# Kernel optimization log

Measured on AMD Instinct MI355X. Metric: run time of the kernel, lower is better.

Reference implementation:

```python
import jax, jax.numpy as jnp
import numpy as np

N = 50000      # nodes
E = 800000     # edges
D_IN = 128     # raw feature dim
H = 96         # hidden_channels
K = 8          # experts
L = 4          # num_layers
C = 40         # classes


def setup_inputs() -> dict:
    key = jax.random.key(0)
    ks = jax.random.split(key, 10)
    stdv = 1.0 / np.sqrt(H)
    inp = {
        'x': jax.random.normal(ks[0], (N, D_IN), dtype=jnp.float32),
        'edge_index': jax.random.randint(ks[1], (2, E), 0, N, dtype=jnp.int64),
        # fcs[0]: Linear(d, hidden); fcs[1]: Linear(hidden, c)
        'fc0_w': jax.random.normal(ks[2], (D_IN, H), dtype=jnp.float32) * 0.05,
        'fc0_b': jnp.zeros((H,), dtype=jnp.float32),
        'fc1_w': jax.random.normal(ks[3], (H, C), dtype=jnp.float32) * 0.05,
        'fc1_b': jnp.zeros((C,), dtype=jnp.float32),
        # context_enc (method='node'): per-layer Linear(hidden, K)
        'ctx_w': jax.random.normal(ks[4], (L, H, K), dtype=jnp.float32) * 0.05,
        'ctx_b': jnp.zeros((L, K), dtype=jnp.float32),
        # GraphMultiConvolution weights: [L, K, hidden, hidden], uniform(-stdv, stdv)
        'conv_w': jax.random.uniform(ks[5], (L, K, H, H), dtype=jnp.float32,
                                     minval=-stdv, maxval=stdv),
    }
    return inp


def reference(x, edge_index, fc0_w, fc0_b, fc1_w, fc1_b, ctx_w, ctx_b, conv_w):
    # eval-mode forward (training=False): no dropout, softmax routing
    row = edge_index[0]
    col = edge_index[1]
    h = jax.nn.relu(x @ fc0_w + fc0_b)                     # [N, H]
    for i in range(L):
        # routing logits and soft expert weights z: [N, K]
        z = jax.nn.softmax(h @ ctx_w[i] + ctx_b[i], axis=-1)
        # spmm aggregation: hi[r] = sum over edges (r, c) of h[c]
        hi = jax.ops.segment_sum(h[col], row, num_segments=N)  # [N, H]
        # K-expert batched matmul: [N, K, H]
        outs = jnp.einsum('nd,kdo->nko', hi, conv_w[i])
        # gumbel/softmax-weighted combine + residual
        out = jnp.einsum('nk,nko->no', z, outs) + h
        h = jax.nn.relu(out)
    return h @ fc1_w + fc1_b                               # [N, C]
```

## Files before the change

kernel.cpp:

```cpp
#include <hip/hip_runtime.h>

#define N_NODES 50000
#define N_EDGES 800000
#define DIN     128
#define H       96
#define K_EXP   8
#define L_LAYERS 4
#define C_OUT   40

typedef _Float16 f16;
typedef f16 f16x2 __attribute__((ext_vector_type(2)));
typedef f16 f16x4 __attribute__((ext_vector_type(4)));
typedef f16 f16x8 __attribute__((ext_vector_type(8)));
typedef float f32x4 __attribute__((ext_vector_type(4)));


#define CONV_TOT (L_LAYERS * K_EXP * H * H)
#define FC0_TOT  (DIN * H)
#define FC1_TOT  (48 * H)
#define CNT_BLOCKS ((N_EDGES + 255) / 256)
#define CVT_BLOCKS ((CONV_TOT + FC0_TOT + FC1_TOT + 255) / 256)

__global__ __launch_bounds__(256) void count_convert(const int* __restrict__ row,
                                                     int* __restrict__ deg,
                                                     int* __restrict__ p,
                                                     const float* __restrict__ conv_w,
                                                     const float* __restrict__ fc0_w,
                                                     const float* __restrict__ fc1_w,
                                                     f16* __restrict__ wfrag,
                                                     f16* __restrict__ fc0t,
                                                     f16* __restrict__ fc1t) {
    int tid = threadIdx.x;
    if ((int)blockIdx.x < CNT_BLOCKS) {
        int i = blockIdx.x * 256 + tid;
        if (i < N_EDGES) p[i] = atomicAdd(&deg[row[i]], 1);
    } else {
        int i = ((int)blockIdx.x - CNT_BLOCKS) * 256 + tid;
        if (i < CONV_TOT) {
            int o = i % H;
            int t = i / H;
            int d = t % H;
            int lk = t / H;
            int ct = o >> 4, lc = o & 15;
            int ks = d >> 5, quad = (d >> 3) & 3, j = d & 7;
            wfrag[(size_t)lk * 9216 + ct * 1536 + ks * 512 + (quad * 16 + lc) * 8 + j] =
                (f16)conv_w[i];
        } else if (i < CONV_TOT + FC0_TOT) {
            int j = i - CONV_TOT;
            int o = j % H, d = j / H;
            fc0t[o * DIN + d] = (f16)fc0_w[j];
        } else if (i < CONV_TOT + FC0_TOT + FC1_TOT) {
            int j = i - CONV_TOT - FC0_TOT;
            int o = j / H, d = j % H;
            fc1t[j] = (o < C_OUT) ? (f16)fc1_w[d * C_OUT + o] : (f16)0.f;
        }
    }
}

__global__ __launch_bounds__(1024) void scanA(const int* __restrict__ deg,
                                              int* __restrict__ rowptr,
                                              int* __restrict__ partial, int n) {
    __shared__ int wsum[16];
    int tid  = threadIdx.x;
    int lane = tid & 63, wid = tid >> 6;
    int idx = blockIdx.x * 1024 + tid;
    int v = (idx < n) ? deg[idx] : 0;
    int s = v;
    #pragma unroll
    for (int off = 1; off < 64; off <<= 1) {
        int t = __shfl_up(s, off, 64);
        if (lane >= off) s += t;
    }
    if (lane == 63) wsum[wid] = s;
    __syncthreads();
    if (wid == 0 && lane < 16) {
        int w = wsum[lane];
        #pragma unroll
        for (int off = 1; off < 16; off <<= 1) {
            int t = __shfl_up(w, off, 16);
            if (lane >= off) w += t;
        }
        wsum[lane] = w;
    }
    __syncthreads();
    int waveoff = (wid == 0) ? 0 : wsum[wid - 1];
    if (idx < n) rowptr[idx + 1] = waveoff + s;
    if (tid == 1023) partial[blockIdx.x] = waveoff + s;
}

__global__ __launch_bounds__(1024) void scanC(int* __restrict__ rowptr,
                                              const int* __restrict__ partial,
                                              int nb, int n) {
    __shared__ int boff_s;
    int tid = threadIdx.x;
    if (tid < 64) {
        int v = 0;
        for (int j = tid; j < (int)blockIdx.x; j += 64) v += partial[j];
        #pragma unroll
        for (int off = 32; off >= 1; off >>= 1) v += __shfl_xor(v, off, 64);
        if (tid == 0) boff_s = v;
    }
    __syncthreads();
    int boff = boff_s;
    int idx = blockIdx.x * 1024 + tid;
    if (idx == 0) rowptr[0] = 0;
    if (idx < n) rowptr[idx + 1] += boff;
}


#define SCT_BLOCKS 1024
#define FPAD 136

__global__ __launch_bounds__(256) void scatter_fc0(const int* __restrict__ row,
                                                   const int* __restrict__ col,
                                                   const int* __restrict__ p,
                                                   const int* __restrict__ rowptr,
                                                   int* __restrict__ csr,
                                                   const float* __restrict__ x,
                                                   const f16* __restrict__ fc0t,
                                                   const float* __restrict__ b,
                                                   f16* __restrict__ h16, int n) {
    __shared__ f16 As[64 * FPAD];
    __shared__ f16 Ws[96 * FPAD];
    int tid = threadIdx.x;
    if ((int)blockIdx.x < SCT_BLOCKS) {
        int stride = SCT_BLOCKS * 256;
        for (int i = blockIdx.x * 256 + tid; i < N_EDGES; i += stride)
            csr[rowptr[row[i]] + p[i]] = col[i];
        return;
    }
    int l = tid & 63, w = tid >> 6;
    int quad = l >> 4, lc = l & 15;
    int row0 = ((int)blockIdx.x - SCT_BLOCKS) * 64;

    for (int t = tid; t < 2048; t += 256) {
        int m = t >> 5, c4 = (t & 31) * 4;
        int gr = row0 + m;
        float4 v = {0.f, 0.f, 0.f, 0.f};
        if (gr < n) v = *(const float4*)(x + (size_t)gr * DIN + c4);
        f16x4 h4 = {(f16)v.x, (f16)v.y, (f16)v.z, (f16)v.w};
        *(f16x4*)&As[m * FPAD + c4] = h4;
    }
    for (int t = tid; t < 1536; t += 256) {
        int o = t >> 4, c8 = (t & 15) * 8;
        *(f16x8*)&Ws[o * FPAD + c8] = *(const f16x8*)(fc0t + o * DIN + c8);
    }
    __syncthreads();

    f16x8 afr[4];
    #pragma unroll
    for (int ks = 0; ks < 4; ks++)
        afr[ks] = *(const f16x8*)&As[(16 * w + lc) * FPAD + ks * 32 + quad * 8];

    f32x4 acc[6] = {};
    #pragma unroll
    for (int ct = 0; ct < 6; ct++) {
        #pragma unroll
        for (int ks = 0; ks < 4; ks++) {
            f16x8 bfr = *(const f16x8*)&Ws[(ct * 16 + lc) * FPAD + ks * 32 + quad * 8];
            acc[ct] = __builtin_amdgcn_mfma_f32_16x16x32_f16(afr[ks], bfr, acc[ct], 0, 0, 0);
        }
    }

    int m0 = 16 * w + quad * 4;
    #pragma unroll
    for (int r = 0; r < 4; r++) {
        int gr = row0 + m0 + r;
        if (gr < n) {
            #pragma unroll
            for (int ct = 0; ct < 6; ct++) {
                int o = ct * 16 + lc;
                h16[(size_t)gr * H + o] = (f16)fmaxf(acc[ct][r] + b[o], 0.f);
            }
        }
    }
}


#define LF_ROWS   64
#define LF_BLOCKS ((N_NODES + LF_ROWS - 1) / LF_ROWS)
#define HPAD      104

#define ACC8(v) { _Pragma("unroll") for (int q = 0; q < 8; q++) acc[q] += (float)(v)[q]; }

__global__ __launch_bounds__(256, 4) void layer_fused(const f16* __restrict__ h16,
                                                      const int* __restrict__ rowptr,
                                                      const int* __restrict__ csr,
                                                      const float* __restrict__ cw,
                                                      const float* __restrict__ cb,
                                                      const f16* __restrict__ wfrag,
                                                      f16* __restrict__ hout16, int n) {
    __shared__ f16 hi_lds[LF_ROWS * HPAD];
    __shared__ f16 Wl[9216];
    __shared__ float ws[H * K_EXP];
    __shared__ f16 z_lds[LF_ROWS * K_EXP];
    __shared__ float bs[K_EXP];

    int tid = threadIdx.x;
    int brow = blockIdx.x * LF_ROWS;

    for (int t = tid; t < H * K_EXP; t += 256) ws[t] = cw[t];
    if (tid < K_EXP) bs[tid] = cb[tid];

    {
        int g = tid >> 4, li = tid & 15;
        bool act = li < 12;
        const f16* hb = h16 + li * 8;
        for (int sub = 0; sub < 4; sub++) {
            int r = brow + g * 4 + sub;
            if (r >= n) break;
            int j = rowptr[r], e = rowptr[r + 1];
            float acc[8] = {};
            int4 qa = *(const int4*)(csr + j);
            int4 qb = *(const int4*)(csr + j + 4);
            while (j + 8 <= e) {
                int4 na = *(const int4*)(csr + j + 8);
                int4 nb = *(const int4*)(csr + j + 12);
                f16x8 v0 = {}, v1 = {}, v2 = {}, v3 = {}, v4 = {}, v5 = {}, v6 = {}, v7 = {};
                if (act) {
                    v0 = *(const f16x8*)(hb + (size_t)qa.x * H);
                    v1 = *(const f16x8*)(hb + (size_t)qa.y * H);
                    v2 = *(const f16x8*)(hb + (size_t)qa.z * H);
                    v3 = *(const f16x8*)(hb + (size_t)qa.w * H);
                    v4 = *(const f16x8*)(hb + (size_t)qb.x * H);
                    v5 = *(const f16x8*)(hb + (size_t)qb.y * H);
                    v6 = *(const f16x8*)(hb + (size_t)qb.z * H);
                    v7 = *(const f16x8*)(hb + (size_t)qb.w * H);
                }
                ACC8(v0) ACC8(v1) ACC8(v2) ACC8(v3)
                ACC8(v4) ACC8(v5) ACC8(v6) ACC8(v7)
                j += 8; qa = na; qb = nb;
            }
            if (j + 4 <= e) {
                f16x8 v0 = {}, v1 = {}, v2 = {}, v3 = {};
                if (act) {
                    v0 = *(const f16x8*)(hb + (size_t)qa.x * H);
                    v1 = *(const f16x8*)(hb + (size_t)qa.y * H);
                    v2 = *(const f16x8*)(hb + (size_t)qa.z * H);
                    v3 = *(const f16x8*)(hb + (size_t)qa.w * H);
                }
                ACC8(v0) ACC8(v1) ACC8(v2) ACC8(v3)
                j += 4; qa = qb;
            }
            int rem = e - j;
            if (rem > 0) {
                f16x8 v0 = {}, v1 = {}, v2 = {};
                if (act) {
                    v0 = *(const f16x8*)(hb + (size_t)qa.x * H);
                    if (rem > 1) v1 = *(const f16x8*)(hb + (size_t)qa.y * H);
                    if (rem > 2) v2 = *(const f16x8*)(hb + (size_t)qa.z * H);
                }
                ACC8(v0)
                if (rem > 1) ACC8(v1)
                if (rem > 2) ACC8(v2)
            }
            if (act) {
                f16x8 o;
                #pragma unroll
                for (int q = 0; q < 8; q++) o[q] = (f16)acc[q];
                *(f16x8*)&hi_lds[(g * 4 + sub) * HPAD + li * 8] = o;
            }
        }
    }

    __syncthreads();
    if (tid < LF_ROWS) {
        int node = brow + tid;
        if (node < n) {
            float acc[K_EXP];
            #pragma unroll
            for (int k = 0; k < K_EXP; k++) acc[k] = bs[k];
            const f16* hr = h16 + (size_t)node * H;
            #pragma unroll 3
            for (int c8 = 0; c8 < 12; c8++) {
                f16x8 v = *(const f16x8*)(hr + c8 * 8);
                #pragma unroll
                for (int j = 0; j < 8; j++) {
                    float hv = (float)v[j];
                    int d = c8 * 8 + j;
                    #pragma unroll
                    for (int k = 0; k < K_EXP; k++) acc[k] += hv * ws[d * K_EXP + k];
                }
            }
            float mx = acc[0];
            #pragma unroll
            for (int k = 1; k < K_EXP; k++) mx = fmaxf(mx, acc[k]);
            float s = 0.f;
            #pragma unroll
            for (int k = 0; k < K_EXP; k++) { acc[k] = __expf(acc[k] - mx); s += acc[k]; }
            float inv = 1.f / s;
            f16x8 zo;
            #pragma unroll
            for (int k = 0; k < K_EXP; k++) zo[k] = (f16)(acc[k] * inv);
            *(f16x8*)&z_lds[tid * K_EXP] = zo;
        }
    }
    __syncthreads();

    int l = tid & 63, w = tid >> 6;
    int quad = l >> 4, lc = l & 15;

    f16x8 afr[3];
    #pragma unroll
    for (int ks = 0; ks < 3; ks++)
        afr[ks] = *(const f16x8*)&hi_lds[(w * 16 + lc) * HPAD + ks * 32 + quad * 8];
    f16x8 zh = *(const f16x8*)&z_lds[(w * 16 + lc) * K_EXP];

    f32x4 acc[6] = {};
    for (int k = 0; k < K_EXP; k++) {
        if (k) __syncthreads();
        const f16* src = wfrag + (size_t)k * 9216;
        for (int t = tid; t < 1152; t += 256)
            *(f16x8*)&Wl[t * 8] = *(const f16x8*)(src + t * 8);
        __syncthreads();

        f16 s = zh[k];
        f16x8 as0 = afr[0] * s, as1 = afr[1] * s, as2 = afr[2] * s;
        #pragma unroll
        for (int ct = 0; ct < 6; ct++) {
            f16x8 b0 = *(const f16x8*)&Wl[ct * 1536 + 0 * 512 + l * 8];
            f16x8 b1 = *(const f16x8*)&Wl[ct * 1536 + 1 * 512 + l * 8];
            f16x8 b2 = *(const f16x8*)&Wl[ct * 1536 + 2 * 512 + l * 8];
            acc[ct] = __builtin_amdgcn_mfma_f32_16x16x32_f16(as0, b0, acc[ct], 0, 0, 0);
            acc[ct] = __builtin_amdgcn_mfma_f32_16x16x32_f16(as1, b1, acc[ct], 0, 0, 0);
            acc[ct] = __builtin_amdgcn_mfma_f32_16x16x32_f16(as2, b2, acc[ct], 0, 0, 0);
        }
    }

    #pragma unroll
    for (int r = 0; r < 4; r++) {
        int gr = brow + w * 16 + quad * 4 + r;
        if (gr < n) {
            #pragma unroll
            for (int ct = 0; ct < 6; ct++) {
                int o = ct * 16 + lc;
                float v = fmaxf(acc[ct][r] + (float)h16[(size_t)gr * H + o], 0.f);
                hout16[(size_t)gr * H + o] = (f16)v;
            }
        }
    }
}


#define APAD 104

__global__ __launch_bounds__(256) void fc1_kernel(const f16* __restrict__ h16,
                                                  const f16* __restrict__ fc1t,
                                                  const float* __restrict__ b,
                                                  float* __restrict__ out, int n) {
    __shared__ f16 As[64 * APAD];
    __shared__ f16 Ws[48 * APAD];
    int tid = threadIdx.x;
    int l = tid & 63, w = tid >> 6;
    int quad = l >> 4, lc = l & 15;
    int row0 = blockIdx.x * 64;

    for (int t = tid; t < 768; t += 256) {
        int m = t / 12, c8 = (t % 12) * 8;
        int gr = row0 + m;
        f16x8 v = {};
        if (gr < n) v = *(const f16x8*)(h16 + (size_t)gr * H + c8);
        *(f16x8*)&As[m * APAD + c8] = v;
    }
    for (int t = tid; t < 576; t += 256) {
        int o = t / 12, c8 = (t % 12) * 8;
        *(f16x8*)&Ws[o * APAD + c8] = *(const f16x8*)(fc1t + o * H + c8);
    }
    __syncthreads();

    f16x8 afr[3];
    #pragma unroll
    for (int ks = 0; ks < 3; ks++)
        afr[ks] = *(const f16x8*)&As[(16 * w + lc) * APAD + ks * 32 + quad * 8];

    f32x4 acc[3] = {};
    #pragma unroll
    for (int ct = 0; ct < 3; ct++) {
        #pragma unroll
        for (int ks = 0; ks < 3; ks++) {
            f16x8 bfr = *(const f16x8*)&Ws[(ct * 16 + lc) * APAD + ks * 32 + quad * 8];
            acc[ct] = __builtin_amdgcn_mfma_f32_16x16x32_f16(afr[ks], bfr, acc[ct], 0, 0, 0);
        }
    }

    int m0 = 16 * w + quad * 4;
    #pragma unroll
    for (int r = 0; r < 4; r++) {
        int gr = row0 + m0 + r;
        if (gr < n) {
            #pragma unroll
            for (int ct = 0; ct < 3; ct++) {
                int o = ct * 16 + lc;
                if (o < C_OUT)
                    out[(size_t)gr * C_OUT + o] = acc[ct][r] + b[o];
            }
        }
    }
}


extern "C" void kernel_launch(void* const* d_in, const int* in_sizes, int n_in,
                              void* d_out, int out_size, void* d_ws, size_t ws_size,
                              hipStream_t stream) {
    const float* x      = (const float*)d_in[0];
    const int*   ei     = (const int*)d_in[1];
    const float* fc0_w  = (const float*)d_in[2];
    const float* fc0_b  = (const float*)d_in[3];
    const float* fc1_w  = (const float*)d_in[4];
    const float* fc1_b  = (const float*)d_in[5];
    const float* ctx_w  = (const float*)d_in[6];
    const float* ctx_b  = (const float*)d_in[7];
    const float* conv_w = (const float*)d_in[8];
    float* out = (float*)d_out;

    const size_t NH = (size_t)N_NODES * H;

    f16*   h16a = (f16*)d_ws;
    f16*   h16b = h16a + NH;
    f16*   wfrag= h16b + NH;
    f16*   fc0t = wfrag + CONV_TOT;
    f16*   fc1t = fc0t + FC0_TOT;
    int* rowptr = (int*)(fc1t + FC1_TOT);
    int* deg    = rowptr + (N_NODES + 1);
    int* csr    = deg + N_NODES;
    int* prank  = csr + N_EDGES;
    int* partial  = prank + N_EDGES;

    const int* row = ei;
    const int* col = ei + N_EDGES;

    hipMemsetAsync(deg, 0, sizeof(int) * N_NODES, stream);

    count_convert<<<CNT_BLOCKS + CVT_BLOCKS, 256, 0, stream>>>(
        row, deg, prank, conv_w, fc0_w, fc1_w, wfrag, fc0t, fc1t);
    int nsb = (N_NODES + 1023) / 1024;
    scanA<<<nsb, 1024, 0, stream>>>(deg, rowptr, partial, N_NODES);
    scanC<<<nsb, 1024, 0, stream>>>(rowptr, partial, nsb, N_NODES);

    int gemm_grid = (N_NODES + 63) / 64;
    scatter_fc0<<<SCT_BLOCKS + gemm_grid, 256, 0, stream>>>(
        row, col, prank, rowptr, csr, x, fc0t, fc0_b, h16a, N_NODES);

    f16* hcur = h16a;
    f16* hnext = h16b;
    for (int i = 0; i < L_LAYERS; i++) {
        layer_fused<<<LF_BLOCKS, 256, 0, stream>>>(
            hcur, rowptr, csr,
            ctx_w + (size_t)i * H * K_EXP, ctx_b + (size_t)i * K_EXP,
            wfrag + (size_t)i * K_EXP * H * H, hnext, N_NODES);
        f16* t = hcur; hcur = hnext; hnext = t;
    }
    fc1_kernel<<<gemm_grid, 256, 0, stream>>>(hcur, fc1t, fc1_b, out, N_NODES);
}
```

Before: 336.8 us.

## Make layer_fused wave-independent: per-wave gather, shuffle softmax, direct global weight loads

Restructures the fused layer kernel so each wavefront handles its own 16 rows end to end. The sparse gather rows are remapped per wave, and the routing softmax is computed by all 64 lanes with cross-quad shuffles instead of a single 64-thread group writing to LDS. Expert weight fragments are read straight from global/L2 instead of being staged through a 9216-element LDS buffer with block-wide barriers per expert. The smaller LDS footprint lets the occupancy hint rise from 4 to 6 blocks, at the cost of repeated global weight traffic per wave and more register pressure from the fully unrolled expert loop.

```diff
diff --git a/kernel.cpp b/kernel.cpp
--- a/kernel.cpp
+++ b/kernel.cpp
@@ -183,7 +183,7 @@
 
 #define ACC8(v) { _Pragma("unroll") for (int q = 0; q < 8; q++) acc[q] += (float)(v)[q]; }
 
-__global__ __launch_bounds__(256, 4) void layer_fused(const f16* __restrict__ h16,
+__global__ __launch_bounds__(256, 6) void layer_fused(const f16* __restrict__ h16,
                                                       const int* __restrict__ rowptr,
                                                       const int* __restrict__ csr,
                                                       const float* __restrict__ cw,
@@ -191,9 +191,7 @@
                                                       const f16* __restrict__ wfrag,
                                                       f16* __restrict__ hout16, int n) {
     __shared__ f16 hi_lds[LF_ROWS * HPAD];
-    __shared__ f16 Wl[9216];
     __shared__ float ws[H * K_EXP];
-    __shared__ f16 z_lds[LF_ROWS * K_EXP];
     __shared__ float bs[K_EXP];
 
     int tid = threadIdx.x;
@@ -201,140 +199,142 @@
 
     for (int t = tid; t < H * K_EXP; t += 256) ws[t] = cw[t];
     if (tid < K_EXP) bs[tid] = cb[tid];
+    __syncthreads();
+
+    int l = tid & 63, w = tid >> 6;
+    int quad = l >> 4, li = l & 15;
+    int wrow = brow + w * 16;
+    if (wrow >= n) return;
 
     {
-        int g = tid >> 4, li = tid & 15;
         bool act = li < 12;
         const f16* hb = h16 + li * 8;
         for (int sub = 0; sub < 4; sub++) {
-            int r = brow + g * 4 + sub;
-            if (r >= n) break;
-            int j = rowptr[r], e = rowptr[r + 1];
+            int r = wrow + quad * 4 + sub;
             float acc[8] = {};
-            int4 qa = *(const int4*)(csr + j);
-            int4 qb = *(const int4*)(csr + j + 4);
-            while (j + 8 <= e) {
-                int4 na = *(const int4*)(csr + j + 8);
-                int4 nb = *(const int4*)(csr + j + 12);
-                f16x8 v0 = {}, v1 = {}, v2 = {}, v3 = {}, v4 = {}, v5 = {}, v6 = {}, v7 = {};
-                if (act) {
-                    v0 = *(const f16x8*)(hb + (size_t)qa.x * H);
-                    v1 = *(const f16x8*)(hb + (size_t)qa.y * H);
-                    v2 = *(const f16x8*)(hb + (size_t)qa.z * H);
-                    v3 = *(const f16x8*)(hb + (size_t)qa.w * H);
-                    v4 = *(const f16x8*)(hb + (size_t)qb.x * H);
-                    v5 = *(const f16x8*)(hb + (size_t)qb.y * H);
-                    v6 = *(const f16x8*)(hb + (size_t)qb.z * H);
-                    v7 = *(const f16x8*)(hb + (size_t)qb.w * H);
+            if (r < n) {
+                int j = rowptr[r], e = rowptr[r + 1];
+                int4 qa = *(const int4*)(csr + j);
+                int4 qb = *(const int4*)(csr + j + 4);
+                while (j + 8 <= e) {
+                    int4 na = *(const int4*)(csr + j + 8);
+                    int4 nb = *(const int4*)(csr + j + 12);
+                    f16x8 v0 = {}, v1 = {}, v2 = {}, v3 = {}, v4 = {}, v5 = {}, v6 = {}, v7 = {};
+                    if (act) {
+                        v0 = *(const f16x8*)(hb + (size_t)qa.x * H);
+                        v1 = *(const f16x8*)(hb + (size_t)qa.y * H);
+                        v2 = *(const f16x8*)(hb + (size_t)qa.z * H);
+                        v3 = *(const f16x8*)(hb + (size_t)qa.w * H);
+                        v4 = *(const f16x8*)(hb + (size_t)qb.x * H);
+                        v5 = *(const f16x8*)(hb + (size_t)qb.y * H);
+                        v6 = *(const f16x8*)(hb + (size_t)qb.z * H);
+                        v7 = *(const f16x8*)(hb + (size_t)qb.w * H);
+                    }
+                    ACC8(v0) ACC8(v1) ACC8(v2) ACC8(v3)
+                    ACC8(v4) ACC8(v5) ACC8(v6) ACC8(v7)
+                    j += 8; qa = na; qb = nb;
                 }
-                ACC8(v0) ACC8(v1) ACC8(v2) ACC8(v3)
-                ACC8(v4) ACC8(v5) ACC8(v6) ACC8(v7)
-                j += 8; qa = na; qb = nb;
-            }
-            if (j + 4 <= e) {
-                f16x8 v0 = {}, v1 = {}, v2 = {}, v3 = {};
-                if (act) {
-                    v0 = *(const f16x8*)(hb + (size_t)qa.x * H);
-                    v1 = *(const f16x8*)(hb + (size_t)qa.y * H);
-                    v2 = *(const f16x8*)(hb + (size_t)qa.z * H);
-                    v3 = *(const f16x8*)(hb + (size_t)qa.w * H);
+                if (j + 4 <= e) {
+                    f16x8 v0 = {}, v1 = {}, v2 = {}, v3 = {};
+                    if (act) {
+                        v0 = *(const f16x8*)(hb + (size_t)qa.x * H);
+                        v1 = *(const f16x8*)(hb + (size_t)qa.y * H);
+                        v2 = *(const f16x8*)(hb + (size_t)qa.z * H);
+                        v3 = *(const f16x8*)(hb + (size_t)qa.w * H);
+                    }
+                    ACC8(v0) ACC8(v1) ACC8(v2) ACC8(v3)
+                    j += 4; qa = qb;
                 }
-                ACC8(v0) ACC8(v1) ACC8(v2) ACC8(v3)
-                j += 4; qa = qb;
-            }
-            int rem = e - j;
-            if (rem > 0) {
-                f16x8 v0 = {}, v1 = {}, v2 = {};
-                if (act) {
-                    v0 = *(const f16x8*)(hb + (size_t)qa.x * H);
-                    if (rem > 1) v1 = *(const f16x8*)(hb + (size_t)qa.y * H);
-                    if (rem > 2) v2 = *(const f16x8*)(hb + (size_t)qa.z * H);
+                int rem = e - j;
+                if (rem > 0) {
+                    f16x8 v0 = {}, v1 = {}, v2 = {};
+                    if (act) {
+                        v0 = *(const f16x8*)(hb + (size_t)qa.x * H);
+                        if (rem > 1) v1 = *(const f16x8*)(hb + (size_t)qa.y * H);
+                        if (rem > 2) v2 = *(const f16x8*)(hb + (size_t)qa.z * H);
+                    }
+                    ACC8(v0)
+                    if (rem > 1) ACC8(v1)
+                    if (rem > 2) ACC8(v2)
                 }
-                ACC8(v0)
-                if (rem > 1) ACC8(v1)
-                if (rem > 2) ACC8(v2)
             }
             if (act) {
                 f16x8 o;
                 #pragma unroll
                 for (int q = 0; q < 8; q++) o[q] = (f16)acc[q];
-                *(f16x8*)&hi_lds[(g * 4 + sub) * HPAD + li * 8] = o;
-            }
-        }
-    }
-
-    __syncthreads();
-    if (tid < LF_ROWS) {
-        int node = brow + tid;
+                *(f16x8*)&hi_lds[(w * 16 + quad * 4 + sub) * HPAD + li * 8] = o;
+            }
+        }
+    }
+
+    float ca[K_EXP];
+    #pragma unroll
+    for (int k = 0; k < K_EXP; k++) ca[k] = 0.f;
+    {
+        int node = wrow + li;
         if (node < n) {
-            float acc[K_EXP];
+            const f16* hr = h16 + (size_t)node * H + quad * 24;
             #pragma unroll
-            for (int k = 0; k < K_EXP; k++) acc[k] = bs[k];
-            const f16* hr = h16 + (size_t)node * H;
-            #pragma unroll 3
-            for (int c8 = 0; c8 < 12; c8++) {
+            for (int c8 = 0; c8 < 3; c8++) {
                 f16x8 v = *(const f16x8*)(hr + c8 * 8);
                 #pragma unroll
-                for (int j = 0; j < 8; j++) {
-                    float hv = (float)v[j];
-                    int d = c8 * 8 + j;
+                for (int jj = 0; jj < 8; jj++) {
+                    float hv = (float)v[jj];
+                    int d = quad * 24 + c8 * 8 + jj;
                     #pragma unroll
-                    for (int k = 0; k < K_EXP; k++) acc[k] += hv * ws[d * K_EXP + k];
+                    for (int k = 0; k < K_EXP; k++) ca[k] += hv * ws[d * K_EXP + k];
                 }
             }
-            float mx = acc[0];
-            #pragma unroll
-            for (int k = 1; k < K_EXP; k++) mx = fmaxf(mx, acc[k]);
-            float s = 0.f;
-            #pragma unroll
-            for (int k = 0; k < K_EXP; k++) { acc[k] = __expf(acc[k] - mx); s += acc[k]; }
-            float inv = 1.f / s;
-            f16x8 zo;
-            #pragma unroll
-            for (int k = 0; k < K_EXP; k++) zo[k] = (f16)(acc[k] * inv);
-            *(f16x8*)&z_lds[tid * K_EXP] = zo;
-        }
-    }
-    __syncthreads();
-
-    int l = tid & 63, w = tid >> 6;
-    int quad = l >> 4, lc = l & 15;
+        }
+    }
+    #pragma unroll
+    for (int k = 0; k < K_EXP; k++) {
+        ca[k] += __shfl_xor(ca[k], 16, 64);
+        ca[k] += __shfl_xor(ca[k], 32, 64);
+        ca[k] += bs[k];
+    }
+    float mx = ca[0];
+    #pragma unroll
+    for (int k = 1; k < K_EXP; k++) mx = fmaxf(mx, ca[k]);
+    float ssum = 0.f;
+    #pragma unroll
+    for (int k = 0; k < K_EXP; k++) { ca[k] = __expf(ca[k] - mx); ssum += ca[k]; }
+    float inv = 1.f / ssum;
+    f16 zh[K_EXP];
+    #pragma unroll
+    for (int k = 0; k < K_EXP; k++) zh[k] = (f16)(ca[k] * inv);
 
     f16x8 afr[3];
     #pragma unroll
     for (int ks = 0; ks < 3; ks++)
-        afr[ks] = *(const f16x8*)&hi_lds[(w * 16 + lc) * HPAD + ks * 32 + quad * 8];
-    f16x8 zh = *(const f16x8*)&z_lds[(w * 16 + lc) * K_EXP];
-
-    f32x4 acc[6] = {};
+        afr[ks] = *(const f16x8*)&hi_lds[(w * 16 + li) * HPAD + ks * 32 + quad * 8];
+
+    f32x4 acc2[6] = {};
+    const f16* wbase = wfrag + (size_t)l * 8;
+    #pragma unroll
     for (int k = 0; k < K_EXP; k++) {
-        if (k) __syncthreads();
-        const f16* src = wfrag + (size_t)k * 9216;
-        for (int t = tid; t < 1152; t += 256)
-            *(f16x8*)&Wl[t * 8] = *(const f16x8*)(src + t * 8);
-        __syncthreads();
-
         f16 s = zh[k];
         f16x8 as0 = afr[0] * s, as1 = afr[1] * s, as2 = afr[2] * s;
+        const f16* wk = wbase + (size_t)k * 9216;
         #pragma unroll
         for (int ct = 0; ct < 6; ct++) {
-            f16x8 b0 = *(const f16x8*)&Wl[ct * 1536 + 0 * 512 + l * 8];
-            f16x8 b1 = *(const f16x8*)&Wl[ct * 1536 + 1 * 512 + l * 8];
-            f16x8 b2 = *(const f16x8*)&Wl[ct * 1536 + 2 * 512 + l * 8];
-            acc[ct] = __builtin_amdgcn_mfma_f32_16x16x32_f16(as0, b0, acc[ct], 0, 0, 0);
-            acc[ct] = __builtin_amdgcn_mfma_f32_16x16x32_f16(as1, b1, acc[ct], 0, 0, 0);
-            acc[ct] = __builtin_amdgcn_mfma_f32_16x16x32_f16(as2, b2, acc[ct], 0, 0, 0);
+            f16x8 b0 = *(const f16x8*)(wk + ct * 1536);
+            f16x8 b1 = *(const f16x8*)(wk + ct * 1536 + 512);
+            f16x8 b2 = *(const f16x8*)(wk + ct * 1536 + 1024);
+            acc2[ct] = __builtin_amdgcn_mfma_f32_16x16x32_f16(as0, b0, acc2[ct], 0, 0, 0);
+            acc2[ct] = __builtin_amdgcn_mfma_f32_16x16x32_f16(as1, b1, acc2[ct], 0, 0, 0);
+            acc2[ct] = __builtin_amdgcn_mfma_f32_16x16x32_f16(as2, b2, acc2[ct], 0, 0, 0);
         }
     }
 
     #pragma unroll
     for (int r = 0; r < 4; r++) {
-        int gr = brow + w * 16 + quad * 4 + r;
+        int gr = wrow + quad * 4 + r;
         if (gr < n) {
             #pragma unroll
             for (int ct = 0; ct < 6; ct++) {
-                int o = ct * 16 + lc;
-                float v = fmaxf(acc[ct][r] + (float)h16[(size_t)gr * H + o], 0.f);
+                int o = ct * 16 + li;
+                float v = fmaxf(acc2[ct][r] + (float)h16[(size_t)gr * H + o], 0.f);
                 hout16[(size_t)gr * H + o] = (f16)v;
             }
         }
```

New measurement: 419.7 us. 24.6% more time.
